# Optimization experiments

Hardware: AMD Instinct MI355X
Metric: run time of the kernel (lower is better)

The kernel has to match this reference:

```python
import jax, jax.numpy as jnp
import numpy as np

B, T, C, H = 2, 1024, 1024, 16
NOPE, ROPED, VD = 32, 64, 32
QLORA, KVLORA = 96, 32
BLK, WIN, KEEP = 16, 256, 256
EPS = 1e-6
SCALE = float(1.0 / np.sqrt(NOPE + ROPED))


def _rope(x):
    # x: [B,H,S,D]; half-split rotation as in apply_rope (chunk into real/imag halves)
    S, D = x.shape[-2], x.shape[-1]
    freqs = 1.0 / (10000.0 ** (jnp.arange(0, D, 2, dtype=jnp.float32) / D))
    f = jnp.arange(S, dtype=jnp.float32)[:, None] * freqs[None, :]
    cos, sin = jnp.cos(f), jnp.sin(f)
    xr, xi = jnp.split(x, 2, axis=-1)
    return jnp.concatenate([xr * cos - xi * sin, xr * sin + xi * cos], -1)


def _rms(x, w):
    return x * jax.lax.rsqrt(jnp.mean(x * x, -1, keepdims=True) + EPS) * w


def _attend(q, k, v, mask=None):
    s = jnp.einsum('bhtd,bhsd->bhts', q, k) * SCALE
    if mask is not None:
        s = jnp.where(mask, s, -1e30)
    return jnp.einsum('bhts,bhsd->bhtd', jax.nn.softmax(s, -1), v)


def _heads(y, d):
    # [B,S,H*d] -> [B,H,S,d]
    return y.reshape(y.shape[0], y.shape[1], H, d).transpose(0, 2, 1, 3)


def setup_inputs() -> dict:
    key = jax.random.key(0)
    ks = jax.random.split(key, 18)
    s = 0.02
    def w(k, shape):
        return jax.random.normal(k, shape, jnp.float32) * s
    return {
        'x': jax.random.normal(ks[0], (B, T, C), jnp.float32),
        'Wcq': w(ks[1], (C, QLORA)), 'qnw': jnp.ones((QLORA,), jnp.float32),
        'Wdqn': w(ks[2], (QLORA, H * NOPE)), 'Wdqr': w(ks[3], (QLORA, H * ROPED)),
        'Wckv': w(ks[4], (C, KVLORA)), 'kvnw': jnp.ones((KVLORA,), jnp.float32),
        'Wdkn': w(ks[5], (KVLORA, H * NOPE)), 'Wdv': w(ks[6], (KVLORA, H * VD)),
        'Wkr': w(ks[7], (C, ROPED)),
        'Wimp': w(ks[8], (C, 1)),
        'Wselk': w(ks[9], (C, H * (ROPED + NOPE))), 'Wselv': w(ks[10], (C, H * VD)),
        'Wwink': w(ks[11], (C, H * (ROPED + NOPE))), 'Wwinv': w(ks[12], (C, H * VD)),
        'Wc1': w(ks[13], (BLK * C, 4 * C)), 'Wc2': w(ks[14], (4 * C, C)),
        'pos_enc': jax.random.normal(ks[15], (1, BLK, C), jnp.float32),
        'Wgate': w(ks[16], (C, 3)), 'Wproj': w(ks[17], (H * VD, C)),
    }


def reference(x, Wcq, qnw, Wdqn, Wdqr, Wckv, kvnw, Wdkn, Wdv, Wkr, Wimp,
              Wselk, Wselv, Wwink, Wwinv, Wc1, Wc2, pos_enc, Wgate, Wproj):
    # --- MLA queries: compress -> RMSNorm -> decompress into nope + rope parts ---
    nq = _rms(x @ Wcq, qnw)
    q_nope = _heads(nq @ Wdqn, NOPE)
    q_rope = _rope(_heads(nq @ Wdqr, ROPED))
    q = jnp.concatenate([q_nope, q_rope], -1)                    # [B,H,T,96]

    # --- branch 1: NSA coarse compression of token blocks, MLA KV decompress ---
    blocks = x.reshape(B, T // BLK, BLK, C) + pos_enc            # intra-block pos enc
    cb = jax.nn.gelu(blocks.reshape(B, T // BLK, BLK * C) @ Wc1, approximate=False) @ Wc2  # [B,NB,C]
    nkv = _rms(cb @ Wckv, kvnw)
    k_nope = _heads(nkv @ Wdkn, NOPE)                            # [B,H,NB,32]
    v1 = _heads(nkv @ Wdv, VD)
    k_rope = _rope(((cb @ Wkr) / H)[:, None])                    # [B,1,NB,64], shared across heads
    k1 = jnp.concatenate([k_nope, jnp.broadcast_to(k_rope, k_nope.shape[:3] + (ROPED,))], -1)
    o1 = _attend(q, k1, v1)                                      # [B,H,T,32]

    # --- branch 2: importance-scored top-k token selection ---
    imp = (x @ Wimp)[..., 0]                                     # [B,T]
    _, idx = jax.lax.top_k(imp, KEEP)
    idx = jnp.sort(idx, -1)                                      # [B,KEEP] sorted
    sel = jnp.take_along_axis(x, idx[:, :, None], axis=1)        # [B,KEEP,C]
    o2 = _attend(q, _heads(sel @ Wselk, ROPED + NOPE), _heads(sel @ Wselv, VD))

    # --- branch 3: causal sliding-window attention ---
    i = jnp.arange(T)[:, None]
    j = jnp.arange(T)[None, :]
    mask = (j <= i) & (i - j < WIN)
    o3 = _attend(q, _heads(x @ Wwink, ROPED + NOPE), _heads(x @ Wwinv, VD), mask)

    # --- per-token gated combination of branches, then output projection ---
    g = jax.nn.softmax(x @ Wgate, -1)                            # [B,T,3]
    outs = [o.transpose(0, 2, 1, 3).reshape(B, T, H * VD) for o in (o1, o2, o3)]
    comb = g[..., 0:1] * outs[0] + g[..., 1:2] * outs[1] + g[..., 2:3] * outs[2]
    return comb @ Wproj                                          # [B,T,C]
```

## Files before the change

### kernel.cpp

```cpp
#include <hip/hip_runtime.h>
#include <hip/hip_bf16.h>
#include <cmath>

#define Bsz 2
#define Tt 1024
#define Cc 1024
#define Hh 16
#define WINd 256
#define KEEPd 256
#define EPSF 1e-6f

typedef __attribute__((ext_vector_type(8))) short bf16x8;
typedef __attribute__((ext_vector_type(4))) float f32x4;
typedef __attribute__((ext_vector_type(4))) float float4_t;
typedef __attribute__((ext_vector_type(2))) unsigned int uint2_t;

static __device__ __forceinline__ float gelu_exact(float v) {
    return 0.5f * v * (1.f + erff(v * 0.70710678118654752f));
}

static __device__ __forceinline__ unsigned int pack2bf(float lo, float hi) {
    unsigned a = __float_as_uint(lo);
    unsigned b = __float_as_uint(hi);
    a = (a + 0x7FFFu + ((a >> 16) & 1u)) >> 16;
    b = (b + 0x7FFFu + ((b >> 16) & 1u)) >> 16;
    return (b << 16) | (a & 0xFFFFu);
}

static __device__ __forceinline__ unsigned short bf16of(float v) {
    unsigned a = __float_as_uint(v);
    a = (a + 0x7FFFu + ((a >> 16) & 1u)) >> 16;
    return (unsigned short)a;
}

__global__ void addpos_kernel(const float* __restrict__ x, const float* __restrict__ pos,
                              float* __restrict__ out) {
    int e = blockIdx.x * 256 + threadIdx.x;
    int row = e >> 14;
    int k = e & 16383;
    int b = row >> 6, nb = row & 63;
    int blk = k >> 10, c = k & 1023;
    int t = nb * 16 + blk;
    out[e] = x[(((long)b * Tt + t) << 10) + c] + pos[(blk << 10) + c];
}

__global__ __launch_bounds__(256) void gemm_mfma(
    const float* __restrict__ A, const float* __restrict__ B, float* __restrict__ C,
    int M, int N, int K, const int* __restrict__ a_rows, int flags)
{
    __shared__ unsigned short As[128 * 40];
    __shared__ unsigned short Bs[128 * 40];
    const int tid = threadIdx.x;
    const int bn = blockIdx.x * 128;
    const int bm = blockIdx.y * 128;
    const int kslice = K / gridDim.z;
    const int k_begin = blockIdx.z * kslice;
    const int k_end = k_begin + kslice;

    const int lane = tid & 63;
    const int w = tid >> 6;
    const int wr = w >> 1, wc = w & 1;
    const int lr = lane & 15, lk = lane >> 4;

    f32x4 acc[4][4];
#pragma unroll
    for (int i = 0; i < 4; i++)
#pragma unroll
        for (int j = 0; j < 4; j++) acc[i][j] = (f32x4){0.f, 0.f, 0.f, 0.f};

    for (int k0 = k_begin; k0 < k_end; k0 += 32) {
#pragma unroll
        for (int l = 0; l < 4; l++) {
            int u = tid + l * 256;
            int row = u >> 3, qq = u & 7;
            int arow = a_rows ? a_rows[bm + row] : bm + row;
            const float4_t va = *(const float4_t*)(A + (long)arow * K + k0 + qq * 4);
            uint2_t p;
            p.x = pack2bf(va.x, va.y);
            p.y = pack2bf(va.z, va.w);
            *(uint2_t*)&As[row * 40 + qq * 4] = p;
        }
#pragma unroll
        for (int l = 0; l < 8; l++) {
            int u = tid + l * 256;
            int kp = u >> 7, n = u & 127;
            int col = bn + n;
            float lo = 0.f, hi = 0.f;
            if (col < N) {
                lo = B[(long)(k0 + 2 * kp) * N + col];
                hi = B[(long)(k0 + 2 * kp + 1) * N + col];
            }
            *(unsigned int*)&Bs[n * 40 + kp * 2] = pack2bf(lo, hi);
        }
        __syncthreads();
        bf16x8 af[4], bfr[4];
#pragma unroll
        for (int i = 0; i < 4; i++)
            af[i] = *(bf16x8*)&As[(wr * 64 + i * 16 + lr) * 40 + lk * 8];
#pragma unroll
        for (int j = 0; j < 4; j++)
            bfr[j] = *(bf16x8*)&Bs[(wc * 64 + j * 16 + lr) * 40 + lk * 8];
#pragma unroll
        for (int i = 0; i < 4; i++)
#pragma unroll
            for (int j = 0; j < 4; j++)
                acc[i][j] = __builtin_amdgcn_mfma_f32_16x16x32_bf16(af[i], bfr[j], acc[i][j], 0, 0, 0);
        __syncthreads();
    }

#pragma unroll
    for (int i = 0; i < 4; i++) {
#pragma unroll
        for (int j = 0; j < 4; j++) {
            int col = bn + wc * 64 + j * 16 + lr;
            if (col < N) {
#pragma unroll
                for (int r = 0; r < 4; r++) {
                    int row = bm + wr * 64 + i * 16 + lk * 4 + r;
                    long idx = (long)row * N + col;
                    if (flags & 2) atomicAdd(&C[idx], acc[i][j][r]);
                    else C[idx] = acc[i][j][r];
                }
            }
        }
    }
}

__global__ void gelu_kernel(float* __restrict__ h) {
    int e = blockIdx.x * 256 + threadIdx.x;
    h[e] = gelu_exact(h[e]);
}

__global__ __launch_bounds__(128) void rms96_kernel(const float* __restrict__ raw,
    const float* __restrict__ wgt, float* __restrict__ out)
{
    int tok = blockIdx.x, tid = threadIdx.x;
    __shared__ float sq[128];
    __shared__ float msh;
    float v = 0.f;
    if (tid < 96) v = raw[tok * 96 + tid];
    sq[tid] = v * v;
    __syncthreads();
    if (tid < 32) {
        float s = sq[tid] + sq[tid + 32] + sq[tid + 64];
        for (int off = 16; off > 0; off >>= 1) s += __shfl_down(s, off);
        if (tid == 0) msh = s * (1.f / 96.f);
    }
    __syncthreads();
    if (tid < 96) out[tok * 96 + tid] = v * rsqrtf(msh + EPSF) * wgt[tid];
}

__global__ __launch_bounds__(256) void rope_q_kernel(const float* __restrict__ qn,
    const float* __restrict__ qr, float* __restrict__ q)
{
    int tok = blockIdx.x, tid = threadIdx.x;
    int t = tok & (Tt - 1);
#pragma unroll
    for (int l = 0; l < 6; l++) {
        int e = tid + l * 256;
        int h = e / 96, d = e % 96;
        float val;
        if (d < 32) val = qn[(long)tok * 512 + h * 32 + d];
        else {
            int dd = d - 32;
            int i = (dd < 32) ? dd : dd - 32;
            float freq = powf(10000.f, -(float)i * (1.f / 32.f));
            float ang = (float)t * freq;
            float sn = sinf(ang), cs = cosf(ang);
            if (dd < 32) val = qr[(long)tok * 1024 + h * 64 + dd] * cs - qr[(long)tok * 1024 + h * 64 + dd + 32] * sn;
            else         val = qr[(long)tok * 1024 + h * 64 + i] * sn + qr[(long)tok * 1024 + h * 64 + dd] * cs;
        }
        q[(long)tok * 1536 + e] = val;
    }
}

__global__ __launch_bounds__(256) void nkv_kernel(const float* __restrict__ cb,
    const float* __restrict__ Wckv, const float* __restrict__ kvnw, float* __restrict__ nkv)
{
    int row = blockIdx.x, tid = threadIdx.x;
    __shared__ float cs[1024];
    __shared__ float red[256];
    __shared__ float vals[32];
    for (int c = tid; c < 1024; c += 256) cs[c] = cb[((long)row << 10) + c];
    __syncthreads();
    int j = tid & 31, g = tid >> 5;
    float acc = 0.f;
    for (int c = g * 128; c < g * 128 + 128; c++) acc += cs[c] * Wckv[c * 32 + j];
    red[tid] = acc; __syncthreads();
    if (tid < 128) red[tid] += red[tid + 128]; __syncthreads();
    if (tid < 64) red[tid] += red[tid + 64]; __syncthreads();
    if (tid < 32) { float v = red[tid] + red[tid + 32]; vals[tid] = v; red[tid] = v * v; }
    __syncthreads();
    if (tid < 16) red[tid] += red[tid + 16]; __syncthreads();
    if (tid < 8) red[tid] += red[tid + 8]; __syncthreads();
    if (tid < 4) red[tid] += red[tid + 4]; __syncthreads();
    if (tid < 2) red[tid] += red[tid + 2]; __syncthreads();
    if (tid < 1) red[0] += red[1]; __syncthreads();
    float mean = red[0] * (1.f / 32.f);
    if (tid < 32) nkv[row * 32 + tid] = vals[tid] * rsqrtf(mean + EPSF) * kvnw[tid];
}

__global__ __launch_bounds__(256) void krope_kernel(const float* __restrict__ cb,
    const float* __restrict__ Wkr, float* __restrict__ krope)
{
    int row = blockIdx.x, tid = threadIdx.x;
    int nb = row & 63;
    __shared__ float cs[1024];
    __shared__ float red[256];
    __shared__ float raw[64];
    for (int c = tid; c < 1024; c += 256) cs[c] = cb[((long)row << 10) + c];
    __syncthreads();
    int d = tid & 63, g = tid >> 6;
    float acc = 0.f;
    for (int c = g * 256; c < g * 256 + 256; c++) acc += cs[c] * Wkr[c * 64 + d];
    red[tid] = acc; __syncthreads();
    if (tid < 128) red[tid] += red[tid + 128]; __syncthreads();
    if (tid < 64) raw[tid] = red[tid] + red[tid + 64];
    __syncthreads();
    if (tid < 64) {
        int dd = tid;
        int i = (dd < 32) ? dd : dd - 32;
        float freq = powf(10000.f, -(float)i * (1.f / 32.f));
        float ang = (float)nb * freq;
        float sn = sinf(ang), c2 = cosf(ang);
        float val;
        if (dd < 32) val = raw[dd] * c2 - raw[dd + 32] * sn;
        else         val = raw[i] * sn + raw[dd] * c2;
        krope[row * 64 + dd] = val * (1.f / 16.f);
    }
}

__global__ void k1_kernel(const float* __restrict__ kn, const float* __restrict__ krope,
                          float* __restrict__ k1) {
    int row = blockIdx.x, tid = threadIdx.x;
#pragma unroll
    for (int l = 0; l < 6; l++) {
        int e = tid + l * 256;
        int h = e / 96, d = e % 96;
        k1[(long)row * 1536 + e] = (d < 32) ? kn[row * 512 + h * 32 + d] : krope[row * 64 + d - 32];
    }
}

__global__ void imp_kernel(const float* __restrict__ x, const float* __restrict__ Wimp,
                           float* __restrict__ imp) {
    int tid = threadIdx.x;
    int w = tid >> 6, lane = tid & 63;
    int tok = blockIdx.x * 4 + w;
    float acc = 0.f;
    for (int c = lane; c < 1024; c += 64) acc += x[((long)tok << 10) + c] * Wimp[c];
    for (int off = 32; off > 0; off >>= 1) acc += __shfl_down(acc, off);
    if (lane == 0) imp[tok] = acc;
}

__global__ __launch_bounds__(256) void topk_kernel(const float* __restrict__ imp,
                                                   int* __restrict__ rows) {
    int b = blockIdx.x, tid = threadIdx.x;
    __shared__ float v[1024];
    __shared__ int flag[1024];
    for (int i = tid; i < 1024; i += 256) v[i] = imp[b * 1024 + i];
    __syncthreads();
    for (int i = tid; i < 1024; i += 256) {
        float vi = v[i]; int r = 0;
        for (int j = 0; j < 1024; j++) {
            float vj = v[j];
            r += (vj > vi) || (vj == vi && j < i);
        }
        flag[i] = (r < KEEPd) ? 1 : 0;
    }
    __syncthreads();
    for (int i = tid; i < 1024; i += 256) {
        if (flag[i]) {
            int p = 0;
            for (int j = 0; j < i; j++) p += flag[j];
            rows[b * KEEPd + p] = b * 1024 + i;
        }
    }
}

__global__ __launch_bounds__(256) void attn_mfma(
    const float* __restrict__ q, const float* __restrict__ Kb, const float* __restrict__ Vb,
    float* __restrict__ o, int SK, int windowed)
{
    const int qt = blockIdx.x;
    const int h  = blockIdx.y;
    const int b  = blockIdx.z;
    const int tid = threadIdx.x;
    const int lane = tid & 63, w = tid >> 6;
    const int lr = lane & 15, lk = lane >> 4;
    const int q0 = qt * 64;
    const float SCALEf = 0.10206207261596577f;

    __shared__ unsigned short Qs[64 * 104];
    __shared__ unsigned short Ks[64 * 104];
    __shared__ unsigned short Vt[32 * 68];
    __shared__ unsigned short Ps[4][16 * 68];

    const float* qbase = q + ((long)(b * Tt + q0)) * 1536 + h * 96;
    for (int u = tid; u < 64 * 24; u += 256) {
        int row = u / 24, c4 = u % 24;
        float4_t v = *(const float4_t*)(qbase + (long)row * 1536 + c4 * 4);
        uint2_t p; p.x = pack2bf(v.x, v.y); p.y = pack2bf(v.z, v.w);
        *(uint2_t*)&Qs[row * 104 + c4 * 4] = p;
    }
    __syncthreads();

    bf16x8 qf[3];
#pragma unroll
    for (int d = 0; d < 3; d++)
        qf[d] = *(bf16x8*)&Qs[(w * 16 + lr) * 104 + d * 32 + lk * 8];

    float mrow[4], ssum[4];
    f32x4 oacc[2];
#pragma unroll
    for (int r = 0; r < 4; r++) { mrow[r] = -1e30f; ssum[r] = 0.f; }
    oacc[0] = (f32x4){0.f,0.f,0.f,0.f};
    oacc[1] = (f32x4){0.f,0.f,0.f,0.f};

    int kb0 = 0, kb1 = SK;
    if (windowed) { kb0 = q0 - 256; if (kb0 < 0) kb0 = 0; kb1 = q0 + 64; }

    for (int kb = kb0; kb < kb1; kb += 64) {
        __syncthreads();
        const float* kbase = Kb + ((long)(b * SK + kb)) * 1536 + h * 96;
        for (int u = tid; u < 64 * 24; u += 256) {
            int row = u / 24, c4 = u % 24;
            float4_t v = *(const float4_t*)(kbase + (long)row * 1536 + c4 * 4);
            uint2_t p; p.x = pack2bf(v.x, v.y); p.y = pack2bf(v.z, v.w);
            *(uint2_t*)&Ks[row * 104 + c4 * 4] = p;
        }
        const float* vbase = Vb + ((long)(b * SK + kb)) * 512 + h * 32;
        for (int u = tid; u < 2048; u += 256) {
            int key = u >> 5, d = u & 31;
            Vt[d * 68 + key] = bf16of(vbase[(long)key * 512 + d]);
        }
        __syncthreads();

        f32x4 s[4];
#pragma unroll
        for (int ct = 0; ct < 4; ct++) {
            s[ct] = (f32x4){0.f,0.f,0.f,0.f};
#pragma unroll
            for (int kk = 0; kk < 3; kk++) {
                bf16x8 kf = *(bf16x8*)&Ks[(ct * 16 + lr) * 104 + kk * 32 + lk * 8];
                s[ct] = __builtin_amdgcn_mfma_f32_16x16x32_bf16(qf[kk], kf, s[ct], 0, 0, 0);
            }
        }

        float cm[4] = {-1e30f, -1e30f, -1e30f, -1e30f};
#pragma unroll
        for (int ct = 0; ct < 4; ct++) {
            int key = kb + ct * 16 + lr;
#pragma unroll
            for (int r = 0; r < 4; r++) {
                float sv = s[ct][r] * SCALEf;
                if (windowed) {
                    int t = q0 + w * 16 + lk * 4 + r;
                    if (!(key <= t && t - key < WINd)) sv = -1e30f;
                }
                s[ct][r] = sv;
                cm[r] = fmaxf(cm[r], sv);
            }
        }
#pragma unroll
        for (int off = 8; off > 0; off >>= 1) {
#pragma unroll
            for (int r = 0; r < 4; r++) cm[r] = fmaxf(cm[r], __shfl_xor(cm[r], off));
        }
        float alpha[4], rs[4];
#pragma unroll
        for (int r = 0; r < 4; r++) {
            float mn = fmaxf(mrow[r], cm[r]);
            alpha[r] = __expf(mrow[r] - mn);
            mrow[r] = mn;
            rs[r] = 0.f;
        }
#pragma unroll
        for (int ct = 0; ct < 4; ct++) {
#pragma unroll
            for (int r = 0; r < 4; r++) {
                float p = (s[ct][r] > -1e29f) ? __expf(s[ct][r] - mrow[r]) : 0.f;
                s[ct][r] = p;
                rs[r] += p;
            }
        }
#pragma unroll
        for (int off = 8; off > 0; off >>= 1) {
#pragma unroll
            for (int r = 0; r < 4; r++) rs[r] += __shfl_xor(rs[r], off);
        }
#pragma unroll
        for (int r = 0; r < 4; r++) ssum[r] = ssum[r] * alpha[r] + rs[r];
#pragma unroll
        for (int dt = 0; dt < 2; dt++)
#pragma unroll
            for (int r = 0; r < 4; r++) oacc[dt][r] *= alpha[r];

#pragma unroll
        for (int ct = 0; ct < 4; ct++)
#pragma unroll
            for (int r = 0; r < 4; r++)
                Ps[w][(lk * 4 + r) * 68 + ct * 16 + lr] = bf16of(s[ct][r]);
        __syncthreads();

        bf16x8 pf[2];
#pragma unroll
        for (int kk = 0; kk < 2; kk++)
            pf[kk] = *(bf16x8*)&Ps[w][lr * 68 + kk * 32 + lk * 8];
#pragma unroll
        for (int dt = 0; dt < 2; dt++) {
#pragma unroll
            for (int kk = 0; kk < 2; kk++) {
                bf16x8 vf = *(bf16x8*)&Vt[(dt * 16 + lr) * 68 + kk * 32 + lk * 8];
                oacc[dt] = __builtin_amdgcn_mfma_f32_16x16x32_bf16(pf[kk], vf, oacc[dt], 0, 0, 0);
            }
        }
    }

#pragma unroll
    for (int dt = 0; dt < 2; dt++) {
#pragma unroll
        for (int r = 0; r < 4; r++) {
            int t = q0 + w * 16 + lk * 4 + r;
            o[((long)(b * Tt + t)) * 512 + h * 32 + dt * 16 + lr] = oacc[dt][r] / ssum[r];
        }
    }
}

__global__ __launch_bounds__(256) void gatecomb_kernel(const float* __restrict__ x,
    const float* __restrict__ Wgate, const float* __restrict__ o1,
    const float* __restrict__ o2, const float* __restrict__ o3, float* __restrict__ comb)
{
    int tok = blockIdx.x, tid = threadIdx.x;
    __shared__ float r0[256], r1[256], r2[256];
    float l0 = 0.f, l1 = 0.f, l2 = 0.f;
    for (int c = tid; c < 1024; c += 256) {
        float xv = x[((long)tok << 10) + c];
        l0 += xv * Wgate[c * 3 + 0];
        l1 += xv * Wgate[c * 3 + 1];
        l2 += xv * Wgate[c * 3 + 2];
    }
    r0[tid] = l0; r1[tid] = l1; r2[tid] = l2; __syncthreads();
    for (int off = 128; off > 0; off >>= 1) {
        if (tid < off) { r0[tid] += r0[tid + off]; r1[tid] += r1[tid + off]; r2[tid] += r2[tid + off]; }
        __syncthreads();
    }
    float a = r0[0], bb = r1[0], cc = r2[0];
    float m = fmaxf(a, fmaxf(bb, cc));
    float e0 = expf(a - m), e1 = expf(bb - m), e2 = expf(cc - m);
    float sinv = 1.f / (e0 + e1 + e2);
    float g0 = e0 * sinv, g1 = e1 * sinv, g2 = e2 * sinv;
    for (int i = tid; i < 512; i += 256) {
        long idx = (long)tok * 512 + i;
        comb[idx] = g0 * o1[idx] + g1 * o2[idx] + g2 * o3[idx];
    }
}

extern "C" void kernel_launch(void* const* d_in, const int* in_sizes, int n_in,
                              void* d_out, int out_size, void* d_ws, size_t ws_size,
                              hipStream_t stream)
{
    const float* x     = (const float*)d_in[0];
    const float* Wcq   = (const float*)d_in[1];
    const float* qnw   = (const float*)d_in[2];
    const float* Wdqn  = (const float*)d_in[3];
    const float* Wdqr  = (const float*)d_in[4];
    const float* Wckv  = (const float*)d_in[5];
    const float* kvnw  = (const float*)d_in[6];
    const float* Wdkn  = (const float*)d_in[7];
    const float* Wdv   = (const float*)d_in[8];
    const float* Wkr   = (const float*)d_in[9];
    const float* Wimp  = (const float*)d_in[10];
    const float* Wselk = (const float*)d_in[11];
    const float* Wselv = (const float*)d_in[12];
    const float* Wwink = (const float*)d_in[13];
    const float* Wwinv = (const float*)d_in[14];
    const float* Wc1   = (const float*)d_in[15];
    const float* Wc2   = (const float*)d_in[16];
    const float* pos   = (const float*)d_in[17];
    const float* Wgate = (const float*)d_in[18];
    const float* Wproj = (const float*)d_in[19];
    float* out = (float*)d_out;

    float* ws = (float*)d_ws;
    size_t off = 0;
    auto alloc = [&](size_t n) { float* p = ws + off; off += n; return p; };
    float* q       = alloc(2048L * 1536);
    float* blocksA = alloc(128L * 16384);
    float* hb      = alloc(128L * 4096);
    float* cb      = alloc(128L * 1024);
    float* nqraw   = alloc(2048L * 96);
    float* nq      = alloc(2048L * 96);
    float* qn      = alloc(2048L * 512);
    float* nkv     = alloc(128L * 32);
    float* kn      = alloc(128L * 512);
    float* v1      = alloc(128L * 512);
    float* krope   = alloc(128L * 64);
    float* k1      = alloc(128L * 1536);
    float* imp     = alloc(2048);
    float* winK    = alloc(2048L * 1536);
    float* winV    = alloc(2048L * 512);
    float* selK    = alloc(512L * 1536);
    float* selV    = alloc(512L * 512);
    float* o1      = alloc(2048L * 512);
    float* o2      = alloc(2048L * 512);
    float* o3      = alloc(2048L * 512);
    float* comb    = alloc(2048L * 512);
    int* rows      = (int*)alloc(512);
    float* qr      = blocksA;

    addpos_kernel<<<8192, 256, 0, stream>>>(x, pos, blocksA);
    hipMemsetAsync(hb, 0, 128L * 4096 * sizeof(float), stream);
    gemm_mfma<<<dim3(32, 1, 8), 256, 0, stream>>>(blocksA, Wc1, hb, 128, 4096, 16384, nullptr, 2);
    gelu_kernel<<<2048, 256, 0, stream>>>(hb);
    hipMemsetAsync(cb, 0, 128L * 1024 * sizeof(float), stream);
    gemm_mfma<<<dim3(8, 1, 8), 256, 0, stream>>>(hb, Wc2, cb, 128, 1024, 4096, nullptr, 2);

    hipMemsetAsync(nqraw, 0, 2048L * 96 * sizeof(float), stream);
    gemm_mfma<<<dim3(1, 16, 4), 256, 0, stream>>>(x, Wcq, nqraw, 2048, 96, 1024, nullptr, 2);
    rms96_kernel<<<2048, 128, 0, stream>>>(nqraw, qnw, nq);
    gemm_mfma<<<dim3(4, 16, 1), 256, 0, stream>>>(nq, Wdqn, qn, 2048, 512, 96, nullptr, 0);
    gemm_mfma<<<dim3(8, 16, 1), 256, 0, stream>>>(nq, Wdqr, qr, 2048, 1024, 96, nullptr, 0);
    rope_q_kernel<<<2048, 256, 0, stream>>>(qn, qr, q);

    nkv_kernel<<<128, 256, 0, stream>>>(cb, Wckv, kvnw, nkv);
    gemm_mfma<<<dim3(4, 1, 1), 256, 0, stream>>>(nkv, Wdkn, kn, 128, 512, 32, nullptr, 0);
    gemm_mfma<<<dim3(4, 1, 1), 256, 0, stream>>>(nkv, Wdv, v1, 128, 512, 32, nullptr, 0);
    krope_kernel<<<128, 256, 0, stream>>>(cb, Wkr, krope);
    k1_kernel<<<128, 256, 0, stream>>>(kn, krope, k1);

    imp_kernel<<<512, 256, 0, stream>>>(x, Wimp, imp);
    topk_kernel<<<2, 256, 0, stream>>>(imp, rows);
    hipMemsetAsync(selK, 0, 512L * 1536 * sizeof(float), stream);
    hipMemsetAsync(selV, 0, 512L * 512 * sizeof(float), stream);
    gemm_mfma<<<dim3(12, 4, 4), 256, 0, stream>>>(x, Wselk, selK, 512, 1536, 1024, rows, 2);
    gemm_mfma<<<dim3(4, 4, 8), 256, 0, stream>>>(x, Wselv, selV, 512, 512, 1024, rows, 2);

    gemm_mfma<<<dim3(12, 16, 1), 256, 0, stream>>>(x, Wwink, winK, 2048, 1536, 1024, nullptr, 0);
    hipMemsetAsync(winV, 0, 2048L * 512 * sizeof(float), stream);
    gemm_mfma<<<dim3(4, 16, 2), 256, 0, stream>>>(x, Wwinv, winV, 2048, 512, 1024, nullptr, 2);

    attn_mfma<<<dim3(16, Hh, Bsz), 256, 0, stream>>>(q, k1, v1, o1, 64, 0);
    attn_mfma<<<dim3(16, Hh, Bsz), 256, 0, stream>>>(q, selK, selV, o2, 256, 0);
    attn_mfma<<<dim3(16, Hh, Bsz), 256, 0, stream>>>(q, winK, winV, o3, Tt, 1);

    gatecomb_kernel<<<2048, 256, 0, stream>>>(x, Wgate, o1, o2, o3, comb);
    gemm_mfma<<<dim3(8, 16, 1), 256, 0, stream>>>(comb, Wproj, out, 2048, 1024, 512, nullptr, 0);
}
```

Measured before the change: 1.683 ms.

## Fuse pos-add and GELU into GEMM loads and raise split-K across GEMMs

The positional-encoding add and block reshaping now happen inside the first compressor GEMM's A-tile load, and GELU is applied inside the second GEMM's A-tile load. This removes the addpos and gelu kernels and the materialized blocksA buffer. Most GEMM launches also get larger split-K factors with atomic accumulation, including winK and the output projection, which now need memsets first. This raises parallelism for small-M GEMMs, at the cost of more atomics, extra memsets, and recomputing GELU once per N-tile.

```diff
diff --git a/kernel.cpp b/kernel.cpp
--- a/kernel.cpp
+++ b/kernel.cpp
@@ -33,20 +33,10 @@
     return (unsigned short)a;
 }
 
-__global__ void addpos_kernel(const float* __restrict__ x, const float* __restrict__ pos,
-                              float* __restrict__ out) {
-    int e = blockIdx.x * 256 + threadIdx.x;
-    int row = e >> 14;
-    int k = e & 16383;
-    int b = row >> 6, nb = row & 63;
-    int blk = k >> 10, c = k & 1023;
-    int t = nb * 16 + blk;
-    out[e] = x[(((long)b * Tt + t) << 10) + c] + pos[(blk << 10) + c];
-}
-
 __global__ __launch_bounds__(256) void gemm_mfma(
     const float* __restrict__ A, const float* __restrict__ B, float* __restrict__ C,
-    int M, int N, int K, const int* __restrict__ a_rows, int flags)
+    int M, int N, int K, const int* __restrict__ a_rows, int flags,
+    const float* __restrict__ posp)
 {
     __shared__ unsigned short As[128 * 40];
     __shared__ unsigned short Bs[128 * 40];
@@ -74,7 +64,21 @@
             int u = tid + l * 256;
             int row = u >> 3, qq = u & 7;
             int arow = a_rows ? a_rows[bm + row] : bm + row;
-            const float4_t va = *(const float4_t*)(A + (long)arow * K + k0 + qq * 4);
+            float4_t va;
+            if (flags & 4) {
+                int col = k0 + qq * 4;
+                int blk = col >> 10, c = col & 1023;
+                long t = ((long)(arow >> 6) << 10) + ((arow & 63) << 4) + blk;
+                va = *(const float4_t*)(A + (t << 10) + c);
+                float4_t pv = *(const float4_t*)(posp + col);
+                va.x += pv.x; va.y += pv.y; va.z += pv.z; va.w += pv.w;
+            } else {
+                va = *(const float4_t*)(A + (long)arow * K + k0 + qq * 4);
+            }
+            if (flags & 8) {
+                va.x = gelu_exact(va.x); va.y = gelu_exact(va.y);
+                va.z = gelu_exact(va.z); va.w = gelu_exact(va.w);
+            }
             uint2_t p;
             p.x = pack2bf(va.x, va.y);
             p.y = pack2bf(va.z, va.w);
@@ -124,11 +128,6 @@
             }
         }
     }
-}
-
-__global__ void gelu_kernel(float* __restrict__ h) {
-    int e = blockIdx.x * 256 + threadIdx.x;
-    h[e] = gelu_exact(h[e]);
 }
 
 __global__ __launch_bounds__(128) void rms96_kernel(const float* __restrict__ raw,
@@ -485,7 +484,7 @@
     size_t off = 0;
     auto alloc = [&](size_t n) { float* p = ws + off; off += n; return p; };
     float* q       = alloc(2048L * 1536);
-    float* blocksA = alloc(128L * 16384);
+    float* qr      = alloc(2048L * 1024);
     float* hb      = alloc(128L * 4096);
     float* cb      = alloc(128L * 1024);
     float* nqraw   = alloc(2048L * 96);
@@ -506,25 +505,22 @@
     float* o3      = alloc(2048L * 512);
     float* comb    = alloc(2048L * 512);
     int* rows      = (int*)alloc(512);
-    float* qr      = blocksA;
-
-    addpos_kernel<<<8192, 256, 0, stream>>>(x, pos, blocksA);
+
     hipMemsetAsync(hb, 0, 128L * 4096 * sizeof(float), stream);
-    gemm_mfma<<<dim3(32, 1, 8), 256, 0, stream>>>(blocksA, Wc1, hb, 128, 4096, 16384, nullptr, 2);
-    gelu_kernel<<<2048, 256, 0, stream>>>(hb);
+    gemm_mfma<<<dim3(32, 1, 32), 256, 0, stream>>>(x, Wc1, hb, 128, 4096, 16384, nullptr, 2 | 4, pos);
     hipMemsetAsync(cb, 0, 128L * 1024 * sizeof(float), stream);
-    gemm_mfma<<<dim3(8, 1, 8), 256, 0, stream>>>(hb, Wc2, cb, 128, 1024, 4096, nullptr, 2);
+    gemm_mfma<<<dim3(8, 1, 32), 256, 0, stream>>>(hb, Wc2, cb, 128, 1024, 4096, nullptr, 2 | 8, nullptr);
 
     hipMemsetAsync(nqraw, 0, 2048L * 96 * sizeof(float), stream);
-    gemm_mfma<<<dim3(1, 16, 4), 256, 0, stream>>>(x, Wcq, nqraw, 2048, 96, 1024, nullptr, 2);
+    gemm_mfma<<<dim3(1, 16, 16), 256, 0, stream>>>(x, Wcq, nqraw, 2048, 96, 1024, nullptr, 2, nullptr);
     rms96_kernel<<<2048, 128, 0, stream>>>(nqraw, qnw, nq);
-    gemm_mfma<<<dim3(4, 16, 1), 256, 0, stream>>>(nq, Wdqn, qn, 2048, 512, 96, nullptr, 0);
-    gemm_mfma<<<dim3(8, 16, 1), 256, 0, stream>>>(nq, Wdqr, qr, 2048, 1024, 96, nullptr, 0);
+    gemm_mfma<<<dim3(4, 16, 1), 256, 0, stream>>>(nq, Wdqn, qn, 2048, 512, 96, nullptr, 0, nullptr);
+    gemm_mfma<<<dim3(8, 16, 1), 256, 0, stream>>>(nq, Wdqr, qr, 2048, 1024, 96, nullptr, 0, nullptr);
     rope_q_kernel<<<2048, 256, 0, stream>>>(qn, qr, q);
 
     nkv_kernel<<<128, 256, 0, stream>>>(cb, Wckv, kvnw, nkv);
-    gemm_mfma<<<dim3(4, 1, 1), 256, 0, stream>>>(nkv, Wdkn, kn, 128, 512, 32, nullptr, 0);
-    gemm_mfma<<<dim3(4, 1, 1), 256, 0, stream>>>(nkv, Wdv, v1, 128, 512, 32, nullptr, 0);
+    gemm_mfma<<<dim3(4, 1, 1), 256, 0, stream>>>(nkv, Wdkn, kn, 128, 512, 32, nullptr, 0, nullptr);
+    gemm_mfma<<<dim3(4, 1, 1), 256, 0, stream>>>(nkv, Wdv, v1, 128, 512, 32, nullptr, 0, nullptr);
     krope_kernel<<<128, 256, 0, stream>>>(cb, Wkr, krope);
     k1_kernel<<<128, 256, 0, stream>>>(kn, krope, k1);
 
@@ -532,17 +528,19 @@
     topk_kernel<<<2, 256, 0, stream>>>(imp, rows);
     hipMemsetAsync(selK, 0, 512L * 1536 * sizeof(float), stream);
     hipMemsetAsync(selV, 0, 512L * 512 * sizeof(float), stream);
-    gemm_mfma<<<dim3(12, 4, 4), 256, 0, stream>>>(x, Wselk, selK, 512, 1536, 1024, rows, 2);
-    gemm_mfma<<<dim3(4, 4, 8), 256, 0, stream>>>(x, Wselv, selV, 512, 512, 1024, rows, 2);
-
-    gemm_mfma<<<dim3(12, 16, 1), 256, 0, stream>>>(x, Wwink, winK, 2048, 1536, 1024, nullptr, 0);
+    gemm_mfma<<<dim3(12, 4, 8), 256, 0, stream>>>(x, Wselk, selK, 512, 1536, 1024, rows, 2, nullptr);
+    gemm_mfma<<<dim3(4, 4, 16), 256, 0, stream>>>(x, Wselv, selV, 512, 512, 1024, rows, 2, nullptr);
+
+    hipMemsetAsync(winK, 0, 2048L * 1536 * sizeof(float), stream);
+    gemm_mfma<<<dim3(12, 16, 2), 256, 0, stream>>>(x, Wwink, winK, 2048, 1536, 1024, nullptr, 2, nullptr);
     hipMemsetAsync(winV, 0, 2048L * 512 * sizeof(float), stream);
-    gemm_mfma<<<dim3(4, 16, 2), 256, 0, stream>>>(x, Wwinv, winV, 2048, 512, 1024, nullptr, 2);
+    gemm_mfma<<<dim3(4, 16, 4), 256, 0, stream>>>(x, Wwinv, winV, 2048, 512, 1024, nullptr, 2, nullptr);
 
     attn_mfma<<<dim3(16, Hh, Bsz), 256, 0, stream>>>(q, k1, v1, o1, 64, 0);
     attn_mfma<<<dim3(16, Hh, Bsz), 256, 0, stream>>>(q, selK, selV, o2, 256, 0);
     attn_mfma<<<dim3(16, Hh, Bsz), 256, 0, stream>>>(q, winK, winV, o3, Tt, 1);
 
     gatecomb_kernel<<<2048, 256, 0, stream>>>(x, Wgate, o1, o2, o3, comb);
-    gemm_mfma<<<dim3(8, 16, 1), 256, 0, stream>>>(comb, Wproj, out, 2048, 1024, 512, nullptr, 0);
-}
+    hipMemsetAsync(out, 0, 2048L * 1024 * sizeof(float), stream);
+    gemm_mfma<<<dim3(8, 16, 2), 256, 0, stream>>>(comb, Wproj, out, 2048, 1024, 512, nullptr, 2, nullptr);
+}
```

After: 1.373 ms. 18.4% less time.
